# Performance work log

Hardware: AMD Instinct MI355X
Metric: run time of the kernel (lower is better)

The kernel has to match this reference:

```python
import jax, jax.numpy as jnp
import numpy as np

N = 50000      # nodes
E = 600000     # edges
D_IN = 128
D = 128        # embedding_size
H = 2 * D      # GENConv MLP hidden (expansion=2, num_layers=2)
L = 6          # gnn_layers
OUT = 2        # out_channels
EPS_MSG = 1e-7   # GENConv message eps
EPS_SM = 1e-16   # PyG softmax denominator eps
LN_EPS = 1e-5


def setup_inputs() -> dict:
    key = jax.random.key(0)
    ks = jax.random.split(key, 18)
    s_in = 1.0 / np.sqrt(D_IN)
    s_d = 1.0 / np.sqrt(D)
    s_h = 1.0 / np.sqrt(H)
    return {
        "x": jax.random.normal(ks[0], (N, D_IN), jnp.float32),
        "edge_index": jax.random.randint(ks[1], (2, E), 0, N, jnp.int64),
        # node encoder
        "enc_W": jax.random.normal(ks[2], (D_IN, D), jnp.float32) * s_in,
        "enc_b": jnp.zeros((D,), jnp.float32),
        # per-layer DeepGCN params (stacked over L layers)
        "ln_g": jnp.ones((L, D), jnp.float32),
        "ln_b": jnp.zeros((L, D), jnp.float32),
        "t": jnp.ones((L,), jnp.float32),  # learnable softmax temperature
        "W1": jax.random.normal(ks[3], (L, D, H), jnp.float32) * s_d,
        "b1": jnp.zeros((L, H), jnp.float32),
        "mln_g": jnp.ones((L, H), jnp.float32),
        "mln_b": jnp.zeros((L, H), jnp.float32),
        "W2": jax.random.normal(ks[4], (L, H, D), jnp.float32) * s_h,
        "b2": jnp.zeros((L, D), jnp.float32),
        # final MLP head (linear_layers=2)
        "lin_W1": jax.random.normal(ks[5], (D, D), jnp.float32) * s_d,
        "lin_b1": jnp.zeros((D,), jnp.float32),
        "lin_W2": jax.random.normal(ks[6], (D, OUT), jnp.float32) * s_d,
        "lin_b2": jnp.zeros((OUT,), jnp.float32),
    }


def _layernorm(h, g, b):
    mu = jnp.mean(h, axis=-1, keepdims=True)
    var = jnp.mean(jnp.square(h - mu), axis=-1, keepdims=True)
    return (h - mu) * jax.lax.rsqrt(var + LN_EPS) * g + b


def _genconv(h, src, dst, t, W1, b1, mg, mb, W2, b2):
    """GENConv with softmax aggregation: gather -> segment softmax -> scatter -> MLP."""
    msg = jax.nn.relu(h[src]) + EPS_MSG            # [E, D]
    scaled = msg * t
    mmax = jax.ops.segment_max(scaled, dst, num_segments=N)  # [N, D]
    mmax = jnp.where(jnp.isfinite(mmax), mmax, 0.0)          # empty segments
    ex = jnp.exp(scaled - mmax[dst])                          # [E, D]
    denom = jax.ops.segment_sum(ex, dst, num_segments=N)     # [N, D]
    alpha = ex / (denom[dst] + EPS_SM)
    agg = jax.ops.segment_sum(msg * alpha, dst, num_segments=N)  # [N, D]
    out = agg + h                                  # root/self term
    z = out @ W1 + b1                              # [N, 2D]
    z = jax.nn.relu(_layernorm(z, mg, mb))
    return z @ W2 + b2                             # [N, D]


def reference(x, edge_index, enc_W, enc_b, ln_g, ln_b, t, W1, b1,
              mln_g, mln_b, W2, b2, lin_W1, lin_b1, lin_W2, lin_b2):
    src, dst = edge_index[0], edge_index[1]
    h = x @ enc_W + enc_b                          # node encoder [N, D]
    for i in range(L):                             # DeepGCNLayer 'res+' blocks
        g = _layernorm(h, ln_g[i], ln_b[i])
        g = jax.nn.relu(g)                         # (dropout: inference no-op)
        g = _genconv(g, src, dst, t[i], W1[i], b1[i], mln_g[i], mln_b[i], W2[i], b2[i])
        h = h + g
    h = jax.nn.relu(h @ lin_W1 + lin_b1)           # head (dropout_rate=None)
    return h @ lin_W2 + lin_b2                     # [N, OUT]
```

## Files before the change

### kernel.cpp

```cpp
#include <hip/hip_runtime.h>

#define NN 50000
#define EE 600000
#define DD 128
#define HH 256
#define LL 6
#define NB 49

typedef _Float16 f16x8 __attribute__((ext_vector_type(8)));
typedef float f32x4 __attribute__((ext_vector_type(4)));

__device__ __forceinline__ float bf2f(unsigned short u){
  unsigned int x = ((unsigned int)u) << 16; float f; __builtin_memcpy(&f, &x, 4); return f;
}
__device__ __forceinline__ unsigned short f2bf(float f){
  unsigned int x; __builtin_memcpy(&x, &f, 4);
  unsigned int lsb = (x >> 16) & 1u; x += 0x7fffu + lsb; return (unsigned short)(x >> 16);
}
__device__ __forceinline__ float wave_sum(float v){
  #pragma unroll
  for (int off = 32; off >= 1; off >>= 1) v += __shfl_xor(v, off, 64);
  return v;
}
__device__ __forceinline__ unsigned short f2h(float f){
  _Float16 h = (_Float16)f; unsigned short u; __builtin_memcpy(&u, &h, 2); return u;
}
__device__ __forceinline__ float h2f(unsigned short u){
  _Float16 h; __builtin_memcpy(&h, &u, 2); return (float)h;
}

__global__ void k_detect(const unsigned short* __restrict__ xh,
                         const unsigned int* __restrict__ ew,
                         int* __restrict__ flags){
  __shared__ int s_bad, s_nz;
  int t = threadIdx.x;
  if (t == 0){ s_bad = 0; s_nz = 0; }
  __syncthreads();
  int bad = 0;
  for (int i = t; i < 512; i += 256){
    unsigned e = (xh[i] >> 7) & 0xffu;
    if (e < 96u || e > 135u) bad = 1;
  }
  if (bad) atomicOr(&s_bad, 1);
  int nz = 0;
  for (int i = t; i < 1024; i += 256)
    if ((i & 1) && ew[i] != 0u) nz = 1;
  if (nz) atomicOr(&s_nz, 1);
  __syncthreads();
  if (t == 0){
    flags[0] = s_bad ? 1 : 0;
    flags[1] = s_nz ? 0 : 1;
  }
}

__global__ void k_cvt_edges(const void* __restrict__ ei, const int* __restrict__ flags,
                            int* __restrict__ s32, int* __restrict__ d32){
  int e = blockIdx.x*256 + threadIdx.x;
  if (e >= EE) return;
  int sv, dv;
  if (flags[1]){
    const long long* p = (const long long*)ei;
    sv = (int)p[e]; dv = (int)p[EE + e];
  } else {
    const int* p = (const int*)ei;
    sv = p[e]; dv = p[EE + e];
  }
  s32[e] = ((unsigned)sv < (unsigned)NN) ? sv : 0;
  d32[e] = ((unsigned)dv < (unsigned)NN) ? dv : 0;
}

__global__ void k_hist(const int* __restrict__ dst, int* __restrict__ deg){
  int e = blockIdx.x*256 + threadIdx.x;
  if (e < EE) atomicAdd(&deg[dst[e]], 1);
}

__global__ void k_blocksum(const int* __restrict__ deg, int* __restrict__ bsum){
  __shared__ int ws[4];
  int t = threadIdx.x, b = blockIdx.x;
  int s = 0;
  int i0 = b*1024 + t*4;
  #pragma unroll
  for (int j=0;j<4;j++){ int i = i0+j; if (i < NN) s += deg[i]; }
  #pragma unroll
  for (int off=32; off>=1; off>>=1) s += __shfl_xor(s, off, 64);
  if ((t&63)==0) ws[t>>6] = s;
  __syncthreads();
  if (t==0) bsum[b] = ws[0]+ws[1]+ws[2]+ws[3];
}

__global__ void k_scanb(const int* __restrict__ bsum, int* __restrict__ boff, int* __restrict__ rowptr){
  int lane = threadIdx.x;
  int v = (lane < NB) ? bsum[lane] : 0;
  int inc = v;
  #pragma unroll
  for (int off=1; off<64; off<<=1){ int u = __shfl_up(inc, off, 64); if (lane>=off) inc += u; }
  if (lane < NB) boff[lane] = inc - v;
  if (lane == 63) rowptr[NN] = inc;
}

__global__ void k_scanscatter(const int* __restrict__ deg, const int* __restrict__ boff,
                              int* __restrict__ rowptr, int* __restrict__ pos){
  __shared__ int ws[4];
  int t = threadIdx.x, b = blockIdx.x;
  int lane = t & 63, wid = t >> 6;
  int i0 = b*1024 + t*4;
  int d[4];
  #pragma unroll
  for (int j=0;j<4;j++){ int i=i0+j; d[j] = (i<NN)? deg[i] : 0; }
  int tot = d[0]+d[1]+d[2]+d[3];
  int inc = tot;
  #pragma unroll
  for (int off=1; off<64; off<<=1){ int u = __shfl_up(inc, off, 64); if (lane>=off) inc += u; }
  if (lane==63) ws[wid] = inc;
  __syncthreads();
  int woff = 0;
  for (int w=0; w<wid; w++) woff += ws[w];
  int base = boff[b] + woff + (inc - tot);
  int pre = 0;
  #pragma unroll
  for (int j=0;j<4;j++){
    int i = i0+j;
    if (i<NN){ rowptr[i] = base + pre; pos[i] = base + pre; }
    pre += d[j];
  }
}

__global__ void k_fill(const int* __restrict__ src, const int* __restrict__ dst,
                       int* __restrict__ pos, int* __restrict__ csr){
  int e = blockIdx.x*256 + threadIdx.x;
  if (e < EE){
    int d = dst[e];
    int p = atomicAdd(&pos[d], 1);
    csr[p] = src[e];
  }
}

__global__ void k_prep_w(const int* __restrict__ flags,
    const void* __restrict__ encW, const void* __restrict__ linW1,
    const void* __restrict__ W1, const void* __restrict__ W2,
    unsigned short* __restrict__ ph, unsigned short* __restrict__ pl)
{
  int idx = blockIdx.x*256 + threadIdx.x;
  int fp32 = flags[0];
  const void* src; int off;
  if (idx < 16384){ int n=idx>>7, k=idx&127; src=encW; off=k*128+n; }
  else if (idx < 32768){ int o=idx-16384; int n=o>>7, k=o&127; src=linW1; off=k*128+n; }
  else if (idx < 229376){ int o=idx-32768; int l=o>>15, r=o&32767; int n=r>>7, k=r&127; src=W1; off=l*32768+k*256+n; }
  else { int o=idx-229376; int l=o>>15, r=o&32767; int n=r>>8, k=r&255; src=W2; off=l*32768+k*128+n; }
  float w = fp32 ? ((const float*)src)[off] : bf2f(((const unsigned short*)src)[off]);
  unsigned short h = f2h(w);
  ph[idx] = h;
  pl[idx] = f2h(w - h2f(h));
}

#define SM_ENCB 0
#define SM_LNG 128
#define SM_LNB 896
#define SM_TV 1664
#define SM_B1 1670
#define SM_MG 3206
#define SM_MB 4742
#define SM_B2 6278
#define SM_LINB1 7046
#define SM_LINW2 7174
#define SM_LINB2 7430
#define SM_TOT 7432
__global__ void k_prep_small(const int* __restrict__ flags,
    const void* s0, const void* s1, const void* s2, const void* s3,
    const void* s4, const void* s5, const void* s6, const void* s7,
    const void* s8, const void* s9, const void* s10, float* __restrict__ out)
{
  int i = blockIdx.x*256 + threadIdx.x;
  if (i >= SM_TOT) return;
  int fp32 = flags[0];
  const void* src; int off;
  if      (i < SM_LNG)  { src=s0;  off=i; }
  else if (i < SM_LNB)  { src=s1;  off=i-SM_LNG; }
  else if (i < SM_TV)   { src=s2;  off=i-SM_LNB; }
  else if (i < SM_B1)   { src=s3;  off=i-SM_TV; }
  else if (i < SM_MG)   { src=s4;  off=i-SM_B1; }
  else if (i < SM_MB)   { src=s5;  off=i-SM_MG; }
  else if (i < SM_B2)   { src=s6;  off=i-SM_MB; }
  else if (i < SM_LINB1){ src=s7;  off=i-SM_B2; }
  else if (i < SM_LINW2){ src=s8;  off=i-SM_LINB1; }
  else if (i < SM_LINB2){ src=s9;  off=i-SM_LINW2; }
  else                  { src=s10; off=i-SM_LINB2; }
  out[i] = fp32 ? ((const float*)src)[off] : bf2f(((const unsigned short*)src)[off]);
}

__device__ __forceinline__ void emit_me(unsigned short* me, int row, int col, float g, float tv){
  float m = g + 1e-7f;
  me[(size_t)row*256 + col] = f2h(m);
  me[(size_t)row*256 + 128 + col] = f2h(__expf(fminf(m*tv, 18.f) - 8.f));
}

template<int EPI>
__global__ __launch_bounds__(256, 4) void k_gemm(const void* __restrict__ Ap,
    const unsigned short* __restrict__ WTh, const unsigned short* __restrict__ WTl,
    const float* __restrict__ bias, float* __restrict__ C,
    int M, const int* __restrict__ flags, int aExt)
{
  __shared__ __align__(16) short lA[64*72];
  __shared__ __align__(16) short lW[128*72];

  const int tid = threadIdx.x, lane = tid & 63, wid = tid >> 6;
  const int mi = lane & 15, q = lane >> 4;
  const int rowb = blockIdx.x * 64;
  const int fp32m = flags[0];

  f32x4 acc[4][2];
  #pragma unroll
  for (int a=0;a<4;a++)
    #pragma unroll
    for (int c=0;c<2;c++){ acc[a][c][0]=0.f; acc[a][c][1]=0.f; acc[a][c][2]=0.f; acc[a][c][3]=0.f; }

  const int nW = fp32m ? 2 : 1;
  for (int pass = 0; pass < nW; ++pass){
    const unsigned short* Wp = pass ? WTl : WTh;
    for (int kc = 0; kc < 2; ++kc){
      {
        const int kv = (tid & 7) * 8, r0 = tid >> 3;
        #pragma unroll
        for (int p = 0; p < 2; ++p){
          int row = p*32 + r0, grow = rowb + row;
          uint4 d = make_uint4(0u,0u,0u,0u);
          if (grow < M){
            if (!aExt){
              d = *(const uint4*)((const unsigned short*)Ap + (size_t)grow*128 + kc*64 + kv);
            } else if (!fp32m){
              uint4 u = *(const uint4*)((const unsigned short*)Ap + (size_t)grow*128 + kc*64 + kv);
              const unsigned short* us = (const unsigned short*)&u;
              unsigned short hh[8];
              #pragma unroll
              for (int c=0;c<8;c++) hh[c] = f2h(bf2f(us[c]));
              d.x = hh[0]|((unsigned)hh[1]<<16); d.y = hh[2]|((unsigned)hh[3]<<16);
              d.z = hh[4]|((unsigned)hh[5]<<16); d.w = hh[6]|((unsigned)hh[7]<<16);
            } else {
              const float* fp = (const float*)Ap + (size_t)grow*128 + kc*64 + kv;
              float4 v0 = *(const float4*)fp, v1 = *(const float4*)(fp+4);
              unsigned short hh[8] = {f2h(v0.x),f2h(v0.y),f2h(v0.z),f2h(v0.w),
                                      f2h(v1.x),f2h(v1.y),f2h(v1.z),f2h(v1.w)};
              d.x = hh[0]|((unsigned)hh[1]<<16); d.y = hh[2]|((unsigned)hh[3]<<16);
              d.z = hh[4]|((unsigned)hh[5]<<16); d.w = hh[6]|((unsigned)hh[7]<<16);
            }
          }
          *(uint4*)&lA[row*72 + kv] = d;
        }
        #pragma unroll
        for (int p = 0; p < 4; ++p){
          int n = p*32 + r0;
          *(uint4*)&lW[n*72 + kv] = *(const uint4*)(Wp + (size_t)n*128 + kc*64 + kv);
        }
      }
      __syncthreads();
      #pragma unroll
      for (int ks = 0; ks < 2; ++ks){
        const int koff = ks*32 + q*8;
        f16x8 af[4], bw[2];
        #pragma unroll
        for (int rt=0; rt<4; rt++) af[rt] = *(const f16x8*)&lA[(rt*16+mi)*72 + koff];
        #pragma unroll
        for (int ct=0; ct<2; ct++) bw[ct] = *(const f16x8*)&lW[(wid*32 + ct*16 + mi)*72 + koff];
        #pragma unroll
        for (int rt=0; rt<4; rt++)
          #pragma unroll
          for (int ct=0; ct<2; ct++)
            acc[rt][ct] = __builtin_amdgcn_mfma_f32_16x16x32_f16(af[rt], bw[ct], acc[rt][ct], 0,0,0);
      }
      __syncthreads();
    }
  }
  #pragma unroll
  for (int ct=0; ct<2; ct++){
    const int col = wid*32 + ct*16 + mi;
    const float bf = bias[col];
    #pragma unroll
    for (int rt=0; rt<4; rt++)
      #pragma unroll
      for (int r=0; r<4; r++){
        int row = rowb + rt*16 + q*4 + r;
        if (row < M){
          float v = acc[rt][ct][r] + bf;
          if (EPI == 1) v = fmaxf(v, 0.f);
          C[(size_t)row*128 + col] = v;
        }
      }
  }
}

__global__ __launch_bounds__(256, 3) void k_gemm1(const unsigned short* __restrict__ Ap,
    const unsigned short* __restrict__ WTh, const unsigned short* __restrict__ WTl,
    const float* __restrict__ bias, const float* __restrict__ gam, const float* __restrict__ bet,
    unsigned short* __restrict__ z, int M, const int* __restrict__ flags)
{
  __shared__ __align__(16) short lA[64*72];
  __shared__ __align__(16) short lW[256*72];
  __shared__ float2 sred[4][64];

  const int tid = threadIdx.x, lane = tid & 63, wid = tid >> 6;
  const int mi = lane & 15, q = lane >> 4;
  const int rowb = blockIdx.x * 64;

  f32x4 acc[4][4];
  #pragma unroll
  for (int a=0;a<4;a++)
    #pragma unroll
    for (int c=0;c<4;c++){ acc[a][c][0]=0.f; acc[a][c][1]=0.f; acc[a][c][2]=0.f; acc[a][c][3]=0.f; }

  const int nW = flags[0] ? 2 : 1;
  for (int pass = 0; pass < nW; ++pass){
    const unsigned short* Wp = pass ? WTl : WTh;
    for (int kc = 0; kc < 2; ++kc){
      {
        const int kv = (tid & 7) * 8, r0 = tid >> 3;
        #pragma unroll
        for (int p = 0; p < 2; ++p){
          int row = p*32 + r0, grow = rowb + row;
          uint4 d = make_uint4(0u,0u,0u,0u);
          if (grow < M) d = *(const uint4*)(Ap + (size_t)grow*128 + kc*64 + kv);
          *(uint4*)&lA[row*72 + kv] = d;
        }
        #pragma unroll
        for (int p = 0; p < 8; ++p){
          int n = p*32 + r0;
          *(uint4*)&lW[n*72 + kv] = *(const uint4*)(Wp + (size_t)n*128 + kc*64 + kv);
        }
      }
      __syncthreads();
      #pragma unroll
      for (int ks = 0; ks < 2; ++ks){
        const int koff = ks*32 + q*8;
        f16x8 af[4], bw[4];
        #pragma unroll
        for (int rt=0; rt<4; rt++) af[rt] = *(const f16x8*)&lA[(rt*16+mi)*72 + koff];
        #pragma unroll
        for (int ct=0; ct<4; ct++) bw[ct] = *(const f16x8*)&lW[(wid*64 + ct*16 + mi)*72 + koff];
        #pragma unroll
        for (int rt=0; rt<4; rt++)
          #pragma unroll
          for (int ct=0; ct<4; ct++)
            acc[rt][ct] = __builtin_amdgcn_mfma_f32_16x16x32_f16(af[rt], bw[ct], acc[rt][ct], 0,0,0);
      }
      __syncthreads();
    }
  }
  #pragma unroll
  for (int ct=0; ct<4; ct++){
    const float bf = bias[wid*64 + ct*16 + mi];
    #pragma unroll
    for (int rt=0; rt<4; rt++)
      #pragma unroll
      for (int r=0; r<4; r++) acc[rt][ct][r] += bf;
  }
  #pragma unroll
  for (int rt=0; rt<4; rt++)
    #pragma unroll
    for (int r=0; r<4; r++){
      float s = 0.f, s2 = 0.f;
      #pragma unroll
      for (int ct=0; ct<4; ct++){ float v = acc[rt][ct][r]; s += v; s2 += v*v; }
      #pragma unroll
      for (int off=1; off<16; off<<=1){ s += __shfl_xor(s, off, 64); s2 += __shfl_xor(s2, off, 64); }
      if (mi == 0) sred[wid][rt*16 + q*4 + r] = make_float2(s, s2);
    }
  __syncthreads();
  #pragma unroll
  for (int rt=0; rt<4; rt++)
    #pragma unroll
    for (int r=0; r<4; r++){
      int rl = rt*16 + q*4 + r;
      float2 t0 = sred[0][rl], t1 = sred[1][rl], t2 = sred[2][rl], t3 = sred[3][rl];
      float s = t0.x + t1.x + t2.x + t3.x;
      float s2 = t0.y + t1.y + t2.y + t3.y;
      float m = s * (1.f/256.f);
      float var = s2 * (1.f/256.f) - m*m;
      float rs = rsqrtf(var + 1e-5f);
      int row = rowb + rl;
      if (row < M){
        #pragma unroll
        for (int ct=0; ct<4; ct++){
          int col = wid*64 + ct*16 + mi;
          float v = (acc[rt][ct][r] - m) * rs * gam[col] + bet[col];
          z[(size_t)row*256 + col] = f2h(fmaxf(v, 0.f));
        }
      }
    }
}

__global__ __launch_bounds__(256, 4) void k_gemm2(const unsigned short* __restrict__ Ap,
    const unsigned short* __restrict__ WTh, const unsigned short* __restrict__ WTl,
    const float* __restrict__ bias, float* __restrict__ h,
    const float* __restrict__ gam, const float* __restrict__ bet,
    const float* __restrict__ tp,
    unsigned short* __restrict__ me, unsigned short* __restrict__ hf,
    int M, const int* __restrict__ flags, int doLN)
{
  __shared__ __align__(16) short lA[64*72];
  __shared__ __align__(16) short lW[128*72];
  __shared__ float2 sred[4][64];

  const int tid = threadIdx.x, lane = tid & 63, wid = tid >> 6;
  const int mi = lane & 15, q = lane >> 4;
  const int rowb = blockIdx.x * 64;
  const float tv = tp[0];

  f32x4 acc[4][2];
  #pragma unroll
  for (int a=0;a<4;a++)
    #pragma unroll
    for (int c=0;c<2;c++){ acc[a][c][0]=0.f; acc[a][c][1]=0.f; acc[a][c][2]=0.f; acc[a][c][3]=0.f; }

  const int nW = flags[0] ? 2 : 1;
  for (int pass = 0; pass < nW; ++pass){
    const unsigned short* Wp = pass ? WTl : WTh;
    for (int kc = 0; kc < 4; ++kc){
      {
        const int kv = (tid & 7) * 8, r0 = tid >> 3;
        #pragma unroll
        for (int p = 0; p < 2; ++p){
          int row = p*32 + r0, grow = rowb + row;
          uint4 d = make_uint4(0u,0u,0u,0u);
          if (grow < M) d = *(const uint4*)(Ap + (size_t)grow*256 + kc*64 + kv);
          *(uint4*)&lA[row*72 + kv] = d;
        }
        #pragma unroll
        for (int p = 0; p < 4; ++p){
          int n = p*32 + r0;
          *(uint4*)&lW[n*72 + kv] = *(const uint4*)(Wp + (size_t)n*256 + kc*64 + kv);
        }
      }
      __syncthreads();
      #pragma unroll
      for (int ks = 0; ks < 2; ++ks){
        const int koff = ks*32 + q*8;
        f16x8 af[4], bw[2];
        #pragma unroll
        for (int rt=0; rt<4; rt++) af[rt] = *(const f16x8*)&lA[(rt*16+mi)*72 + koff];
        #pragma unroll
        for (int ct=0; ct<2; ct++) bw[ct] = *(const f16x8*)&lW[(wid*32 + ct*16 + mi)*72 + koff];
        #pragma unroll
        for (int rt=0; rt<4; rt++)
          #pragma unroll
          for (int ct=0; ct<2; ct++)
            acc[rt][ct] = __builtin_amdgcn_mfma_f32_16x16x32_f16(af[rt], bw[ct], acc[rt][ct], 0,0,0);
      }
      __syncthreads();
    }
  }
  #pragma unroll
  for (int ct=0; ct<2; ct++){
    const int col = wid*32 + ct*16 + mi;
    const float bf = bias[col];
    #pragma unroll
    for (int rt=0; rt<4; rt++)
      #pragma unroll
      for (int r=0; r<4; r++){
        int row = rowb + rt*16 + q*4 + r;
        if (row < M){
          float hv = acc[rt][ct][r] + bf + h[(size_t)row*128 + col];
          h[(size_t)row*128 + col] = hv;
          acc[rt][ct][r] = hv;
        }
      }
  }
  if (!doLN){
    #pragma unroll
    for (int ct=0; ct<2; ct++){
      const int col = wid*32 + ct*16 + mi;
      #pragma unroll
      for (int rt=0; rt<4; rt++)
        #pragma unroll
        for (int r=0; r<4; r++){
          int row = rowb + rt*16 + q*4 + r;
          if (row < M) hf[(size_t)row*128 + col] = f2h(acc[rt][ct][r]);
        }
    }
    return;
  }
  #pragma unroll
  for (int rt=0; rt<4; rt++)
    #pragma unroll
    for (int r=0; r<4; r++){
      float s = 0.f, s2 = 0.f;
      #pragma unroll
      for (int ct=0; ct<2; ct++){ float v = acc[rt][ct][r]; s += v; s2 += v*v; }
      #pragma unroll
      for (int off=1; off<16; off<<=1){ s += __shfl_xor(s, off, 64); s2 += __shfl_xor(s2, off, 64); }
      if (mi == 0) sred[wid][rt*16 + q*4 + r] = make_float2(s, s2);
    }
  __syncthreads();
  #pragma unroll
  for (int rt=0; rt<4; rt++)
    #pragma unroll
    for (int r=0; r<4; r++){
      int rl = rt*16 + q*4 + r;
      float2 t0 = sred[0][rl], t1 = sred[1][rl], t2 = sred[2][rl], t3 = sred[3][rl];
      float s = t0.x + t1.x + t2.x + t3.x;
      float s2 = t0.y + t1.y + t2.y + t3.y;
      float m = s * (1.f/128.f);
      float var = s2 * (1.f/128.f) - m*m;
      float rs = rsqrtf(var + 1e-5f);
      int row = rowb + rl;
      if (row < M){
        #pragma unroll
        for (int ct=0; ct<2; ct++){
          int col = wid*32 + ct*16 + mi;
          float g = fmaxf((acc[rt][ct][r] - m) * rs * gam[col] + bet[col], 0.f);
          emit_me(me, row, col, g, tv);
        }
      }
    }
}

__global__ __launch_bounds__(256,4) void k_preln0(const float* __restrict__ h,
    const float* __restrict__ gam, const float* __restrict__ bet,
    const float* __restrict__ tp, unsigned short* __restrict__ me)
{
  int wid = threadIdx.x >> 6, lane = threadIdx.x & 63;
  int row = blockIdx.x*4 + wid;
  float tv = tp[0];
  float2 v = ((const float2*)(h + (size_t)row*DD))[lane];
  float mean = wave_sum(v.x+v.y) * (1.f/128.f);
  float d0 = v.x-mean, d1 = v.y-mean;
  float var = wave_sum(d0*d0 + d1*d1) * (1.f/128.f);
  float rs = rsqrtf(var + 1e-5f);
  float o0 = fmaxf(d0*rs*gam[2*lane]   + bet[2*lane],   0.f);
  float o1 = fmaxf(d1*rs*gam[2*lane+1] + bet[2*lane+1], 0.f);
  emit_me(me, row, 2*lane,   o0, tv);
  emit_me(me, row, 2*lane+1, o1, tv);
}

__global__ __launch_bounds__(256,4) void k_agg(
    const unsigned short* __restrict__ me,
    const int* __restrict__ rowptr, const int* __restrict__ csr,
    unsigned short* __restrict__ obf)
{
  int wid = threadIdx.x>>6, lane = threadIdx.x&63;
  int node = blockIdx.x*4 + wid;
  int st = rowptr[node], en = rowptr[node+1];
  int quad = lane >> 4, fi = lane & 15;
  float l[8], ac[8];
  #pragma unroll
  for (int f=0; f<8; f++){ l[f]=0.f; ac[f]=0.f; }
  for (int base = st; base < en; base += 64){
    int cnt = min(64, en - base);
    int sv = (lane < cnt) ? csr[base + lane] : NN;
    for (int j = 0; j < cnt; j += 4){
      int s = __shfl(sv, j + quad, 64);
      const unsigned short* mer = me + (size_t)s*256 + fi*8;
      f16x8 mh = *(const f16x8*)(mer);
      f16x8 eh = *(const f16x8*)(mer + 128);
      #pragma unroll
      for (int f=0; f<8; f++){
        float ef = (float)eh[f];
        l[f] += ef;
        ac[f] = fmaf((float)mh[f], ef, ac[f]);
      }
    }
  }
  #pragma unroll
  for (int off=16; off<=32; off<<=1)
    #pragma unroll
    for (int f=0; f<8; f++){ l[f] += __shfl_xor(l[f], off, 64); ac[f] += __shfl_xor(ac[f], off, 64); }
  if (quad == 0){
    f16x8 mh = *(const f16x8*)(me + (size_t)node*256 + fi*8);
    bool has = en > st;
    unsigned short o[8];
    #pragma unroll
    for (int f=0; f<8; f++){
      float a = has ? (ac[f] / (l[f] + 1e-16f)) : 0.f;
      o[f] = f2h(((float)mh[f] - 1e-7f) + a);
    }
    uint4 w;
    w.x = o[0]|((unsigned)o[1]<<16); w.y = o[2]|((unsigned)o[3]<<16);
    w.z = o[4]|((unsigned)o[5]<<16); w.w = o[6]|((unsigned)o[7]<<16);
    *(uint4*)(obf + (size_t)node*DD + fi*8) = w;
  }
}

__global__ __launch_bounds__(256,4) void k_head2(const float* __restrict__ u,
    const float* __restrict__ w, const float* __restrict__ b,
    void* __restrict__ out, const int* __restrict__ flags)
{
  int wid = threadIdx.x>>6, lane = threadIdx.x&63;
  int row = blockIdx.x*4 + wid;
  const float* ur = u + (size_t)row*DD;
  float u0 = ur[lane], u1 = ur[lane+64];
  float s0 = u0*w[lane*2+0] + u1*w[(lane+64)*2+0];
  float s1 = u0*w[lane*2+1] + u1*w[(lane+64)*2+1];
  s0 = wave_sum(s0); s1 = wave_sum(s1);
  if (lane == 0){
    float o0 = s0 + b[0], o1 = s1 + b[1];
    if (flags[0]){
      ((float*)out)[row*2+0] = o0;
      ((float*)out)[row*2+1] = o1;
    } else {
      ((unsigned short*)out)[row*2+0] = f2bf(o0);
      ((unsigned short*)out)[row*2+1] = f2bf(o1);
    }
  }
}

extern "C" void kernel_launch(void* const* d_in, const int* in_sizes, int n_in,
                              void* d_out, int out_size, void* d_ws, size_t ws_size,
                              hipStream_t stream)
{
  (void)in_sizes; (void)n_in; (void)out_size; (void)ws_size;
  char* ws = (char*)d_ws;
  size_t off = 0;
  auto alloc = [&](size_t bytes) -> char* {
    char* p = ws + off;
    off = (off + bytes + 255) & ~(size_t)255;
    return p;
  };
  int* flags  = (int*)alloc(256);
  float* sm   = (float*)alloc(SM_TOT*4);
  unsigned short* planeH = (unsigned short*)alloc(425984*2);
  unsigned short* planeL = (unsigned short*)alloc(425984*2);
  int* src32  = (int*)alloc((size_t)EE*4);
  int* dst32  = (int*)alloc((size_t)EE*4);
  int* deg    = (int*)alloc((size_t)NN*4);
  int* pos    = (int*)alloc((size_t)NN*4);
  int* rowptr = (int*)alloc((size_t)(NN+1)*4);
  int* csr    = (int*)alloc((size_t)EE*4);
  int* bsum   = (int*)alloc(64*4);
  int* boff   = (int*)alloc(64*4);
  float* h    = (float*)alloc((size_t)NN*128*4);
  unsigned short* z    = (unsigned short*)alloc((size_t)NN*256*2);
  unsigned short* me   = (unsigned short*)alloc((size_t)(NN+1)*256*2);
  unsigned short* obf  = (unsigned short*)alloc((size_t)NN*128*2);
  unsigned short* hf   = (unsigned short*)alloc((size_t)NN*128*2);
  float* ob   = (float*)alloc((size_t)NN*128*4);

  k_detect<<<1,256,0,stream>>>((const unsigned short*)d_in[0], (const unsigned int*)d_in[1], flags);
  k_cvt_edges<<<(EE+255)/256,256,0,stream>>>(d_in[1], flags, src32, dst32);
  hipMemsetAsync(deg, 0, (size_t)NN*4, stream);
  hipMemsetAsync(me + (size_t)NN*256, 0, 512, stream);
  k_hist<<<(EE+255)/256,256,0,stream>>>(dst32, deg);
  k_blocksum<<<NB,256,0,stream>>>(deg, bsum);
  k_scanb<<<1,64,0,stream>>>(bsum, boff, rowptr);
  k_scanscatter<<<NB,256,0,stream>>>(deg, boff, rowptr, pos);
  k_fill<<<(EE+255)/256,256,0,stream>>>(src32, dst32, pos, csr);
  k_prep_w<<<1664,256,0,stream>>>(flags, d_in[2], d_in[13], d_in[7], d_in[11], planeH, planeL);
  k_prep_small<<<30,256,0,stream>>>(flags, d_in[3], d_in[4], d_in[5], d_in[6], d_in[8],
                                    d_in[9], d_in[10], d_in[12], d_in[14], d_in[15], d_in[16], sm);

  const int GB = (NN + 63)/64;
  k_gemm<0><<<GB,256,0,stream>>>((const void*)d_in[0], planeH + 0, planeL + 0,
                                 sm + SM_ENCB, h, NN, flags, 1);
  k_preln0<<<NN/4,256,0,stream>>>(h, sm + SM_LNG, sm + SM_LNB, sm + SM_TV, me);
  for (int i = 0; i < LL; ++i){
    k_agg<<<NN/4,256,0,stream>>>(me, rowptr, csr, obf);
    k_gemm1<<<GB,256,0,stream>>>(obf, planeH + 32768 + i*32768, planeL + 32768 + i*32768,
                                 sm + SM_B1 + i*256, sm + SM_MG + i*256, sm + SM_MB + i*256,
                                 z, NN, flags);
    int nl = (i+1 < LL) ? (i+1) : 0;
    k_gemm2<<<GB,256,0,stream>>>(z, planeH + 229376 + i*32768, planeL + 229376 + i*32768,
                                 sm + SM_B2 + i*128, h,
                                 sm + SM_LNG + nl*128, sm + SM_LNB + nl*128,
                                 sm + SM_TV + nl,
                                 me, hf, NN, flags, (i+1 < LL) ? 1 : 0);
  }
  k_gemm<1><<<GB,256,0,stream>>>((const void*)hf, planeH + 16384, planeL + 16384,
                                 sm + SM_LINB1, ob, NN, flags, 0);
  k_head2<<<NN/4,256,0,stream>>>(ob, sm + SM_LINW2, sm + SM_LINB2, d_out, flags);
}
```

Baseline: 896.7 us.

## Store residual stream in fp16 and unroll aggregation gather by two

The fp32 residual h buffer is replaced with an fp16 buffer that is read and written by the encoder GEMM, the pre-LN kernel and the gemm2 epilogue. The separate hf copy for the head disappears because the head reads h16 directly. The aggregation loop now issues two neighbour gathers per iteration to expose more memory-level parallelism, and the empty-segment branch is dropped. This halves residual traffic, but the residual accumulates in fp16 over six layers, which risks precision loss.

```diff
diff --git a/kernel.cpp b/kernel.cpp
--- a/kernel.cpp
+++ b/kernel.cpp
@@ -197,7 +197,7 @@
 template<int EPI>
 __global__ __launch_bounds__(256, 4) void k_gemm(const void* __restrict__ Ap,
     const unsigned short* __restrict__ WTh, const unsigned short* __restrict__ WTl,
-    const float* __restrict__ bias, float* __restrict__ C,
+    const float* __restrict__ bias, void* __restrict__ Cv,
     int M, const int* __restrict__ flags, int aExt)
 {
   __shared__ __align__(16) short lA[64*72];
@@ -282,7 +282,8 @@
         if (row < M){
           float v = acc[rt][ct][r] + bf;
           if (EPI == 1) v = fmaxf(v, 0.f);
-          C[(size_t)row*128 + col] = v;
+          if (EPI == 3) ((unsigned short*)Cv)[(size_t)row*128 + col] = f2h(v);
+          else          ((float*)Cv)[(size_t)row*128 + col] = v;
         }
       }
   }
@@ -389,10 +390,10 @@
 
 __global__ __launch_bounds__(256, 4) void k_gemm2(const unsigned short* __restrict__ Ap,
     const unsigned short* __restrict__ WTh, const unsigned short* __restrict__ WTl,
-    const float* __restrict__ bias, float* __restrict__ h,
+    const float* __restrict__ bias, unsigned short* __restrict__ h16,
     const float* __restrict__ gam, const float* __restrict__ bet,
     const float* __restrict__ tp,
-    unsigned short* __restrict__ me, unsigned short* __restrict__ hf,
+    unsigned short* __restrict__ me,
     int M, const int* __restrict__ flags, int doLN)
 {
   __shared__ __align__(16) short lA[64*72];
@@ -457,26 +458,13 @@
       for (int r=0; r<4; r++){
         int row = rowb + rt*16 + q*4 + r;
         if (row < M){
-          float hv = acc[rt][ct][r] + bf + h[(size_t)row*128 + col];
-          h[(size_t)row*128 + col] = hv;
+          float hv = acc[rt][ct][r] + bf + h2f(h16[(size_t)row*128 + col]);
+          h16[(size_t)row*128 + col] = f2h(hv);
           acc[rt][ct][r] = hv;
         }
       }
   }
-  if (!doLN){
-    #pragma unroll
-    for (int ct=0; ct<2; ct++){
-      const int col = wid*32 + ct*16 + mi;
-      #pragma unroll
-      for (int rt=0; rt<4; rt++)
-        #pragma unroll
-        for (int r=0; r<4; r++){
-          int row = rowb + rt*16 + q*4 + r;
-          if (row < M) hf[(size_t)row*128 + col] = f2h(acc[rt][ct][r]);
-        }
-    }
-    return;
-  }
+  if (!doLN) return;
   #pragma unroll
   for (int rt=0; rt<4; rt++)
     #pragma unroll
@@ -512,16 +500,18 @@
     }
 }
 
-__global__ __launch_bounds__(256,4) void k_preln0(const float* __restrict__ h,
+__global__ __launch_bounds__(256,4) void k_preln0(const unsigned short* __restrict__ h16,
     const float* __restrict__ gam, const float* __restrict__ bet,
     const float* __restrict__ tp, unsigned short* __restrict__ me)
 {
   int wid = threadIdx.x >> 6, lane = threadIdx.x & 63;
   int row = blockIdx.x*4 + wid;
   float tv = tp[0];
-  float2 v = ((const float2*)(h + (size_t)row*DD))[lane];
-  float mean = wave_sum(v.x+v.y) * (1.f/128.f);
-  float d0 = v.x-mean, d1 = v.y-mean;
+  unsigned u = ((const unsigned*)(h16 + (size_t)row*DD))[lane];
+  float v0 = h2f((unsigned short)(u & 0xffffu));
+  float v1 = h2f((unsigned short)(u >> 16));
+  float mean = wave_sum(v0+v1) * (1.f/128.f);
+  float d0 = v0-mean, d1 = v1-mean;
   float var = wave_sum(d0*d0 + d1*d1) * (1.f/128.f);
   float rs = rsqrtf(var + 1e-5f);
   float o0 = fmaxf(d0*rs*gam[2*lane]   + bet[2*lane],   0.f);
@@ -545,16 +535,30 @@
   for (int base = st; base < en; base += 64){
     int cnt = min(64, en - base);
     int sv = (lane < cnt) ? csr[base + lane] : NN;
-    for (int j = 0; j < cnt; j += 4){
-      int s = __shfl(sv, j + quad, 64);
-      const unsigned short* mer = me + (size_t)s*256 + fi*8;
-      f16x8 mh = *(const f16x8*)(mer);
-      f16x8 eh = *(const f16x8*)(mer + 128);
-      #pragma unroll
-      for (int f=0; f<8; f++){
-        float ef = (float)eh[f];
-        l[f] += ef;
-        ac[f] = fmaf((float)mh[f], ef, ac[f]);
+    for (int j = 0; j < cnt; j += 8){
+      int s0i = __shfl(sv, j + quad, 64);
+      int s1i = __shfl(sv, j + 4 + quad, 64);
+      bool two = (j + 4) < cnt;
+      const unsigned short* mer0 = me + (size_t)s0i*256 + fi*8;
+      f16x8 mh0 = *(const f16x8*)(mer0);
+      f16x8 eh0 = *(const f16x8*)(mer0 + 128);
+      if (two){
+        const unsigned short* mer1 = me + (size_t)s1i*256 + fi*8;
+        f16x8 mh1 = *(const f16x8*)(mer1);
+        f16x8 eh1 = *(const f16x8*)(mer1 + 128);
+        #pragma unroll
+        for (int f=0; f<8; f++){
+          l[f]  = fmaf((float)eh0[f], 1.f, l[f]);
+          ac[f] = fmaf((float)mh0[f], (float)eh0[f], ac[f]);
+          l[f]  = fmaf((float)eh1[f], 1.f, l[f]);
+          ac[f] = fmaf((float)mh1[f], (float)eh1[f], ac[f]);
+        }
+      } else {
+        #pragma unroll
+        for (int f=0; f<8; f++){
+          l[f]  = fmaf((float)eh0[f], 1.f, l[f]);
+          ac[f] = fmaf((float)mh0[f], (float)eh0[f], ac[f]);
+        }
       }
     }
   }
@@ -564,11 +568,10 @@
     for (int f=0; f<8; f++){ l[f] += __shfl_xor(l[f], off, 64); ac[f] += __shfl_xor(ac[f], off, 64); }
   if (quad == 0){
     f16x8 mh = *(const f16x8*)(me + (size_t)node*256 + fi*8);
-    bool has = en > st;
     unsigned short o[8];
     #pragma unroll
     for (int f=0; f<8; f++){
-      float a = has ? (ac[f] / (l[f] + 1e-16f)) : 0.f;
+      float a = ac[f] / (l[f] + 1e-16f);
       o[f] = f2h(((float)mh[f] - 1e-7f) + a);
     }
     uint4 w;
@@ -625,11 +628,10 @@
   int* csr    = (int*)alloc((size_t)EE*4);
   int* bsum   = (int*)alloc(64*4);
   int* boff   = (int*)alloc(64*4);
-  float* h    = (float*)alloc((size_t)NN*128*4);
+  unsigned short* h16 = (unsigned short*)alloc((size_t)NN*128*2);
   unsigned short* z    = (unsigned short*)alloc((size_t)NN*256*2);
   unsigned short* me   = (unsigned short*)alloc((size_t)(NN+1)*256*2);
   unsigned short* obf  = (unsigned short*)alloc((size_t)NN*128*2);
-  unsigned short* hf   = (unsigned short*)alloc((size_t)NN*128*2);
   float* ob   = (float*)alloc((size_t)NN*128*4);
 
   k_detect<<<1,256,0,stream>>>((const unsigned short*)d_in[0], (const unsigned int*)d_in[1], flags);
@@ -646,9 +648,9 @@
                                     d_in[9], d_in[10], d_in[12], d_in[14], d_in[15], d_in[16], sm);
 
   const int GB = (NN + 63)/64;
-  k_gemm<0><<<GB,256,0,stream>>>((const void*)d_in[0], planeH + 0, planeL + 0,
-                                 sm + SM_ENCB, h, NN, flags, 1);
-  k_preln0<<<NN/4,256,0,stream>>>(h, sm + SM_LNG, sm + SM_LNB, sm + SM_TV, me);
+  k_gemm<3><<<GB,256,0,stream>>>((const void*)d_in[0], planeH + 0, planeL + 0,
+                                 sm + SM_ENCB, (void*)h16, NN, flags, 1);
+  k_preln0<<<NN/4,256,0,stream>>>(h16, sm + SM_LNG, sm + SM_LNB, sm + SM_TV, me);
   for (int i = 0; i < LL; ++i){
     k_agg<<<NN/4,256,0,stream>>>(me, rowptr, csr, obf);
     k_gemm1<<<GB,256,0,stream>>>(obf, planeH + 32768 + i*32768, planeL + 32768 + i*32768,
@@ -656,12 +658,12 @@
                                  z, NN, flags);
     int nl = (i+1 < LL) ? (i+1) : 0;
     k_gemm2<<<GB,256,0,stream>>>(z, planeH + 229376 + i*32768, planeL + 229376 + i*32768,
-                                 sm + SM_B2 + i*128, h,
+                                 sm + SM_B2 + i*128, h16,
                                  sm + SM_LNG + nl*128, sm + SM_LNB + nl*128,
                                  sm + SM_TV + nl,
-                                 me, hf, NN, flags, (i+1 < LL) ? 1 : 0);
-  }
-  k_gemm<1><<<GB,256,0,stream>>>((const void*)hf, planeH + 16384, planeL + 16384,
-                                 sm + SM_LINB1, ob, NN, flags, 0);
+                                 me, NN, flags, (i+1 < LL) ? 1 : 0);
+  }
+  k_gemm<1><<<GB,256,0,stream>>>((const void*)h16, planeH + 16384, planeL + 16384,
+                                 sm + SM_LINB1, (void*)ob, NN, flags, 0);
   k_head2<<<NN/4,256,0,stream>>>(ob, sm + SM_LINW2, sm + SM_LINB2, d_out, flags);
 }
```

New measurement: 884.1 us. About the same (-1.4%).
